# Kernel optimization log

Hardware: AMD Instinct MI355X
Metric: run time of the kernel (lower is better)

The kernel has to match this reference:

```python
import jax, jax.numpy as jnp
import numpy as np

H = 16  # num_attention_heads


def setup_inputs() -> dict:
    key = jax.random.key(0)
    ks = jax.random.split(key, 4)
    B, S, D = 2, 2048, 1024
    hidden_states = jax.random.normal(ks[0], (B, S, D), dtype=jnp.float32)
    attention_mask = jnp.zeros((B, 1, 1, S), dtype=jnp.float32)
    scale = 1.0 / np.sqrt(D)
    Wq = jax.random.normal(ks[1], (D, D), dtype=jnp.float32) * scale
    Wk = jax.random.normal(ks[2], (D, D), dtype=jnp.float32) * scale
    Wv = jax.random.normal(ks[3], (D, D), dtype=jnp.float32) * scale
    bq = jnp.zeros((D,), dtype=jnp.float32)
    bk = jnp.zeros((D,), dtype=jnp.float32)
    bv = jnp.zeros((D,), dtype=jnp.float32)
    return {"hidden_states": hidden_states, "attention_mask": attention_mask,
            "Wq": Wq, "bq": bq, "Wk": Wk, "bk": bk, "Wv": Wv, "bv": bv}


def reference(hidden_states, attention_mask, Wq, bq, Wk, bk, Wv, bv):
    B, S, D = hidden_states.shape
    Dh = D // H

    def proj(W, b):
        # torch Linear: x @ W.T + b ; reshape to [B, H, S, Dh]
        y = jnp.einsum('bsd,ed->bse', hidden_states, W) + b
        return y.reshape(B, S, H, Dh).transpose(0, 2, 1, 3)

    q = proj(Wq, bq)
    k = proj(Wk, bk)
    v = proj(Wv, bv)

    scores = jnp.einsum('bhqd,bhkd->bhqk', q, k) / jnp.sqrt(jnp.float32(Dh))
    scores = scores + attention_mask  # additive mask broadcast [B,1,1,S]
    probs = jax.nn.softmax(scores, axis=-1)  # [B,H,Sq,Sk]
    out_attention_scores = probs.sum(axis=-2).sum(axis=-2)  # [B, Sk]
    # dropout prob = 0 (eval) -> identity
    context = jnp.einsum('bhqk,bhkd->bhqd', probs, v)
    context = context.transpose(0, 2, 1, 3).reshape(B, S, D)
    return context, out_attention_scores
```

## Files before the change

kernel.cpp:

```cpp
#include <hip/hip_runtime.h>
#include <hip/hip_bf16.h>
#include <stdint.h>

typedef unsigned short u16;
typedef __attribute__((ext_vector_type(8))) unsigned short u16x8;
typedef __attribute__((ext_vector_type(4))) unsigned short u16x4;
typedef __attribute__((ext_vector_type(8))) __bf16 bf16x8;
typedef __attribute__((ext_vector_type(4))) float f32x4;
typedef __attribute__((ext_vector_type(16))) float f32x16;

#define LOG2E 1.44269504088896340736f

#if defined(__has_builtin)
#if __has_builtin(__builtin_amdgcn_exp2f)
#define EXP2(x) __builtin_amdgcn_exp2f(x)
#endif
#endif
#ifndef EXP2
#define EXP2(x) exp2f(x)
#endif

__device__ __forceinline__ f32x4 mfma16(u16x8 a, u16x8 b, f32x4 c) {
  return __builtin_amdgcn_mfma_f32_16x16x32_bf16(
      __builtin_bit_cast(bf16x8, a), __builtin_bit_cast(bf16x8, b), c, 0, 0, 0);
}

__device__ __forceinline__ f32x16 mfma32(u16x8 a, u16x8 b, f32x16 c) {
  return __builtin_amdgcn_mfma_f32_32x32x16_bf16(
      __builtin_bit_cast(bf16x8, a), __builtin_bit_cast(bf16x8, b), c, 0, 0, 0);
}

__device__ __forceinline__ u16 f2bf(float f) {
  unsigned u = __builtin_bit_cast(unsigned, f);
  return (u16)((u + 0x7fffu + ((u >> 16) & 1u)) >> 16);
}

__device__ __forceinline__ unsigned cvtpk(float a, float b) {
  unsigned r;
  asm volatile("v_cvt_pk_bf16_f32 %0, %1, %2" : "=v"(r) : "v"(a), "v"(b));
  return r;
}

__device__ __forceinline__ void pswap(unsigned& a, unsigned& b) {
  asm volatile("v_permlane32_swap_b32 %0, %1" : "+v"(a), "+v"(b));
}

__device__ __forceinline__ void gload_lds16(const void* g, void* l) {
  __builtin_amdgcn_global_load_lds(
      (__attribute__((address_space(1))) void*)const_cast<void*>(g),
      (__attribute__((address_space(3))) void*)l, 16, 0, 0);
}

template<int N> __device__ __forceinline__ void vmwait() {
  __builtin_amdgcn_sched_barrier(0);
  asm volatile("s_waitcnt vmcnt(%0)" :: "n"(N) : "memory");
  __builtin_amdgcn_sched_barrier(0);
}

#define SWZ(row, colbyte) ((((row) * 128) + (colbyte)) ^ (((row) & 7) << 4))

__global__ void cast_f32_bf16(const float* __restrict__ src, u16* __restrict__ dst, int n4) {
  int i = blockIdx.x * blockDim.x + threadIdx.x;
  if (i < n4) {
    f32x4 v = ((const f32x4*)src)[i];
    u16x4 o;
    o[0] = f2bf(v[0]); o[1] = f2bf(v[1]); o[2] = f2bf(v[2]); o[3] = f2bf(v[3]);
    ((u16x4*)dst)[i] = o;
  }
}

__global__ void cast3_f32_bf16(const float* __restrict__ s0, const float* __restrict__ s1,
                               const float* __restrict__ s2, u16* __restrict__ dst) {
  const int seg = blockIdx.x >> 10;
  const int i = (blockIdx.x & 1023) * blockDim.x + threadIdx.x;
  const float* src = (seg == 0) ? s0 : ((seg == 1) ? s1 : s2);
  f32x4 v = ((const f32x4*)src)[i];
  u16x4 o;
  o[0] = f2bf(v[0]); o[1] = f2bf(v[1]); o[2] = f2bf(v[2]); o[3] = f2bf(v[3]);
  ((u16x4*)(dst + (size_t)seg * 1048576))[i] = o;
}

__global__ __launch_bounds__(256) void gemm_qkv(
    const u16* __restrict__ A, const u16* __restrict__ Bm,
    const float* __restrict__ bq, const float* __restrict__ bk, const float* __restrict__ bv,
    u16* __restrict__ Qb, u16* __restrict__ Kb, u16* __restrict__ VTb) {
  __shared__ __align__(16) u16 Asm[3][4096];
  __shared__ __align__(16) u16 Bsm[3][4096];
  const int tid = threadIdx.x;
  const int wave = tid >> 6, lane = tid & 63;
  const int lq = lane & 15, lg = lane >> 4;
  const int wr = wave >> 1, wc = wave & 1;
  const int lin = blockIdx.y * 24 + blockIdx.x;
  const int wg = (lin & 7) * 96 + (lin >> 3);
  const int m0 = (wg / 24) * 128, n0 = (wg % 24) * 128;

  f32x4 zero = {0.f, 0.f, 0.f, 0.f};
  f32x4 acc[4][4];
#pragma unroll
  for (int mi = 0; mi < 4; ++mi)
#pragma unroll
    for (int ni = 0; ni < 4; ++ni) acc[mi][ni] = zero;

  auto stage = [&](int kt, int buf) {
    const int k0 = kt * 32;
#pragma unroll
    for (int c = 0; c < 2; ++c) {
      const int idx = wave * 2 + c;
      const u16* ga = A + (size_t)(m0 + idx * 16 + (lane >> 2)) * 1024 + k0 + (lane & 3) * 8;
      gload_lds16(ga, (char*)&Asm[buf][0] + idx * 1024);
      const u16* gb = Bm + (size_t)(n0 + idx * 16 + (lane >> 2)) * 1024 + k0 + (lane & 3) * 8;
      gload_lds16(gb, (char*)&Bsm[buf][0] + idx * 1024);
    }
  };

  stage(0, 0);
  stage(1, 1);
  for (int kt = 0; kt < 32; ++kt) {
    if (kt < 31) vmwait<4>(); else vmwait<0>();
    __builtin_amdgcn_s_barrier();
    if (kt + 2 < 32) stage(kt + 2, (kt + 2) % 3);
    const int cur = kt % 3;

    __builtin_amdgcn_s_setprio(1);
    u16x8 af[4], bfr[4];
#pragma unroll
    for (int mi = 0; mi < 4; ++mi)
      af[mi] = *(const u16x8*)&Asm[cur][(wr * 64 + mi * 16 + lq) * 32 + lg * 8];
#pragma unroll
    for (int ni = 0; ni < 4; ++ni)
      bfr[ni] = *(const u16x8*)&Bsm[cur][(wc * 64 + ni * 16 + lq) * 32 + lg * 8];
#pragma unroll
    for (int mi = 0; mi < 4; ++mi)
#pragma unroll
      for (int ni = 0; ni < 4; ++ni)
        acc[mi][ni] = mfma16(af[mi], bfr[ni], acc[mi][ni]);
    __builtin_amdgcn_s_setprio(0);
  }

  const int which = n0 >> 10;
  const float* bias = (which == 0) ? bq : ((which == 1) ? bk : bv);
  const float scl = (which == 0) ? (0.125f * LOG2E) : 1.0f;
#pragma unroll
  for (int mi = 0; mi < 4; ++mi) {
    const int m = m0 + wr * 64 + mi * 16 + lg * 4;
    const int bb = m >> 11;
    const int s = m & 2047;
#pragma unroll
    for (int ni = 0; ni < 4; ++ni) {
      const int n = n0 + wc * 64 + ni * 16 + lq;
      const int d = n & 1023;
      const int h = d >> 6, dh = d & 63;
      const float bi = bias[d];
#pragma unroll
      for (int r = 0; r < 4; ++r) {
        float v = (acc[mi][ni][r] + bi) * scl;
        if (which == 2)
          VTb[(((size_t)bb * 16 + h) * 64 + dh) * 2048 + (size_t)(s + r)] = f2bf(v);
        else {
          u16* dst = (which == 0) ? Qb : Kb;
          dst[(((size_t)bb * 16 + h) * 2048 + (size_t)(s + r)) * 64 + dh] = f2bf(v);
        }
      }
    }
  }
}

__global__ __launch_bounds__(512) void attn_pair(
    const u16* __restrict__ Qb, const u16* __restrict__ Kb, const u16* __restrict__ VTb,
    const float* __restrict__ maskg, float* __restrict__ out_ctx, float* __restrict__ winv) {
  __shared__ __align__(16) u16 Kl[2][2][4096];
  __shared__ __align__(16) u16 VTl[2][2][4096];

  const int tid = threadIdx.x;
  const int w = tid >> 6, lane = tid & 63;
  const int l31 = lane & 31, h = lane >> 5;
  const int hf = w >> 2, p = w & 3;
  const int bid = (blockIdx.x & 7) * 64 + (blockIdx.x >> 3);
  const int qt = bid & 15, bh = bid >> 4;
  const int b = bh >> 4, hh = bh & 15;
  const int qw = qt * 128 + p * 32;
  const int kt0 = hf * 16;

  const u16* qp = Qb + ((size_t)bh * 2048 + qw + l31) * 64 + h * 8;
  u16x8 qa[4];
#pragma unroll
  for (int dq = 0; dq < 4; ++dq) qa[dq] = *(const u16x8*)(qp + dq * 16);

  const char* Kbase = (const char*)(Kb + (size_t)bh * 2048 * 64);
  const char* VTbase = (const char*)(VTb + (size_t)bh * 64 * 2048);
  const float* mbase = maskg + b * 2048;

  const int t8 = tid & 255;
  const int srow = t8 >> 3;
  const int scol = ((t8 & 7) * 16) ^ ((srow & 7) << 4);
  auto stage = [&](int kt, int buf) {
    const char* ksrc = Kbase + (size_t)(kt * 64) * 128;
    char* kd = (char*)&Kl[hf][buf][0] + (w & 3) * 1024;
    gload_lds16(ksrc + (size_t)srow * 128 + scol, kd);
    gload_lds16(ksrc + (size_t)(srow + 32) * 128 + scol, kd + 4096);
    const char* vsrc = VTbase + (size_t)kt * 128;
    char* vd = (char*)&VTl[hf][buf][0] + (w & 3) * 1024;
    gload_lds16(vsrc + (size_t)srow * 4096 + scol, vd);
    gload_lds16(vsrc + (size_t)(srow + 32) * 4096 + scol, vd + 4096);
  };

  f32x16 accpv[2];
#pragma unroll
  for (int db = 0; db < 2; ++db)
#pragma unroll
    for (int r = 0; r < 16; ++r) accpv[db][r] = 0.f;
  float l_l = 0.f;

  stage(kt0, 0);
  for (int j = 0; j < 16; ++j) {
    const int kt = kt0 + j;
    vmwait<0>();
    __builtin_amdgcn_s_barrier();
    const int cur = j & 1;
    const char* Kt = (const char*)&Kl[hf][cur][0];
    const char* Vt = (const char*)&VTl[hf][cur][0];

    __builtin_amdgcn_s_setprio(1);
#pragma unroll
    for (int kb = 0; kb < 2; ++kb) {
      f32x16 s;
#pragma unroll
      for (int r = 0; r < 16; ++r) s[r] = 0.f;
#pragma unroll
      for (int dq = 0; dq < 4; ++dq) {
        const u16x8 ka = *(const u16x8*)(Kt + SWZ(kb * 32 + l31, dq * 32 + h * 16));
        s = mfma32(ka, qa[dq], s);
      }
      float pv[16];
#pragma unroll
      for (int g = 0; g < 4; ++g) {
        const f32x4 mv = *(const f32x4*)(mbase + kt * 64 + kb * 32 + g * 8 + h * 4);
#pragma unroll
        for (int j2 = 0; j2 < 4; ++j2)
          pv[g * 4 + j2] = EXP2(fmaf(mv[j2], LOG2E, s[g * 4 + j2]));
      }
      l_l += ((pv[0] + pv[1]) + (pv[2] + pv[3])) + ((pv[4] + pv[5]) + (pv[6] + pv[7])) +
             ((pv[8] + pv[9]) + (pv[10] + pv[11])) + ((pv[12] + pv[13]) + (pv[14] + pv[15]));
      unsigned a01 = cvtpk(pv[0], pv[1]), a23 = cvtpk(pv[2], pv[3]);
      unsigned a45 = cvtpk(pv[4], pv[5]), a67 = cvtpk(pv[6], pv[7]);
      unsigned b01 = cvtpk(pv[8], pv[9]), b23 = cvtpk(pv[10], pv[11]);
      unsigned b45 = cvtpk(pv[12], pv[13]), b67 = cvtpk(pv[14], pv[15]);
      pswap(a01, a45); pswap(a23, a67);
      pswap(b01, b45); pswap(b23, b67);
      uint4 f1 = {a01, a23, a45, a67};
      uint4 f2 = {b01, b23, b45, b67};
      u16x8 pf[2] = {__builtin_bit_cast(u16x8, f1), __builtin_bit_cast(u16x8, f2)};
#pragma unroll
      for (int ks2 = 0; ks2 < 2; ++ks2) {
#pragma unroll
        for (int db = 0; db < 2; ++db) {
          const u16x8 vt = *(const u16x8*)(Vt + SWZ(db * 32 + l31, kb * 64 + ks2 * 32 + h * 16));
          accpv[db] = mfma32(pf[ks2], vt, accpv[db]);
        }
      }
    }
    __builtin_amdgcn_s_setprio(0);
    __builtin_amdgcn_sched_barrier(0);
    if (j + 1 < 16) stage(kt0 + j + 1, cur ^ 1);
  }

  l_l += __shfl_xor(l_l, 32);

  __syncthreads();
  float* pairctx = (float*)&Kl[0][0][0];
  float* pairl   = (float*)&VTl[0][0][0];
  if (hf == 1) {
#pragma unroll
    for (int db = 0; db < 2; ++db)
#pragma unroll
      for (int r = 0; r < 16; ++r) {
        const int q = (r & 3) + (r >> 2) * 8 + h * 4;
        pairctx[p * 2048 + q * 64 + db * 32 + l31] = accpv[db][r];
      }
    if (h == 0) pairl[p * 32 + l31] = l_l;
  }
  __syncthreads();
  if (hf == 0) {
    const float lt = l_l + pairl[p * 32 + l31];
    const float il = 1.0f / lt;
    if (h == 0) winv[bh * 2048 + qw + l31] = il;
#pragma unroll
    for (int r = 0; r < 16; ++r) {
      const int q = (r & 3) + (r >> 2) * 8 + h * 4;
      const float ilr = __shfl(il, q);
      const size_t row = (size_t)(b * 2048 + qw + q) * 1024 + hh * 64;
      out_ctx[row + l31] =
          (accpv[0][r] + pairctx[p * 2048 + q * 64 + l31]) * ilr;
      out_ctx[row + 32 + l31] =
          (accpv[1][r] + pairctx[p * 2048 + q * 64 + 32 + l31]) * ilr;
    }
  }
}

__global__ __launch_bounds__(256) void colsum_kernel(
    const u16* __restrict__ Qb, const u16* __restrict__ Kb,
    const float* __restrict__ maskg, const float* __restrict__ winv,
    float* __restrict__ out_cs) {
  __shared__ __align__(16) u16 Ql[3][4096];

  const int tid = threadIdx.x;
  const int w = tid >> 6, lane = tid & 63;
  const int lq = lane & 15, lg = lane >> 4;
  const int bid = (blockIdx.x & 7) * 128 + (blockIdx.x >> 3);
  const int ktile = bid & 15, qh = (bid >> 4) & 1, bh = bid >> 5;
  const int b = bh >> 4;
  const int kbase = ktile * 128 + w * 32;
  const int q0t = qh * 16;

  const u16* kp0 = Kb + ((size_t)bh * 2048 + kbase + lq) * 64 + lg * 8;
  const u16* kp1 = kp0 + 16 * 64;
  const u16x8 kb00 = *(const u16x8*)kp0, kb01 = *(const u16x8*)(kp0 + 32);
  const u16x8 kb10 = *(const u16x8*)kp1, kb11 = *(const u16x8*)(kp1 + 32);
  const float mvl0 = maskg[b * 2048 + kbase + lq] * LOG2E;
  const float mvl1 = maskg[b * 2048 + kbase + 16 + lq] * LOG2E;
  const float* wbase = winv + bh * 2048;
  const char* Qbase = (const char*)(Qb + (size_t)bh * 2048 * 64);

  const int r0 = tid >> 3;
  const int scol = ((tid & 7) * 16) ^ ((r0 & 7) << 4);
  auto stageQ = [&](int qt, int buf) {
    const char* src = Qbase + (size_t)(qt * 64) * 128;
    char* d = (char*)&Ql[buf][0] + w * 1024;
    gload_lds16(src + (size_t)r0 * 128 + scol, d);
    gload_lds16(src + (size_t)(r0 + 32) * 128 + scol, d + 4096);
  };

  float c0 = 0.f, c1 = 0.f;
  stageQ(q0t, 0);
  stageQ(q0t + 1, 1);
  for (int j = 0; j < 16; ++j) {
    const int qt = q0t + j;
    if (j < 15) vmwait<2>(); else vmwait<0>();
    __builtin_amdgcn_s_barrier();
    const char* Qt = (const char*)&Ql[j % 3][0];
    __builtin_amdgcn_s_setprio(1);
#pragma unroll
    for (int chunk = 0; chunk < 4; ++chunk) {
      const u16x8 qf0 = *(const u16x8*)(Qt + SWZ(chunk * 16 + lq, lg * 16));
      const u16x8 qf1 = *(const u16x8*)(Qt + SWZ(chunk * 16 + lq, 64 + lg * 16));
      f32x4 z = {0.f, 0.f, 0.f, 0.f};
      f32x4 s0 = mfma16(qf0, kb00, z);
      s0 = mfma16(qf1, kb01, s0);
      f32x4 s1 = mfma16(qf0, kb10, z);
      s1 = mfma16(qf1, kb11, s1);
      const f32x4 wv = *(const f32x4*)(wbase + qt * 64 + chunk * 16 + lg * 4);
#pragma unroll
      for (int r = 0; r < 4; ++r) {
        c0 += EXP2(s0[r] + mvl0) * wv[r];
        c1 += EXP2(s1[r] + mvl1) * wv[r];
      }
    }
    __builtin_amdgcn_s_setprio(0);
    __builtin_amdgcn_sched_barrier(0);
    if (j + 2 < 16) stageQ(q0t + j + 2, (j + 2) % 3);
  }
  c0 += __shfl_xor(c0, 16); c0 += __shfl_xor(c0, 32);
  c1 += __shfl_xor(c1, 16); c1 += __shfl_xor(c1, 32);
  if (lg == 0) {
    atomicAdd(&out_cs[b * 2048 + kbase + lq], c0);
    atomicAdd(&out_cs[b * 2048 + kbase + 16 + lq], c1);
  }
}

extern "C" void kernel_launch(void* const* d_in, const int* in_sizes, int n_in,
                              void* d_out, int out_size, void* d_ws, size_t ws_size,
                              hipStream_t stream) {
  (void)in_sizes; (void)n_in; (void)out_size; (void)ws_size;
  const float* X    = (const float*)d_in[0];
  const float* mask = (const float*)d_in[1];
  const float* Wq   = (const float*)d_in[2];
  const float* bq   = (const float*)d_in[3];
  const float* Wk   = (const float*)d_in[4];
  const float* bk   = (const float*)d_in[5];
  const float* Wv   = (const float*)d_in[6];
  const float* bv   = (const float*)d_in[7];
  float* out = (float*)d_out;

  char* ws = (char*)d_ws;
  u16* Xb   = (u16*)(ws);
  u16* Wcat = (u16*)(ws + 8388608);
  u16* Qb   = (u16*)(ws + 14680064);
  u16* Kb   = (u16*)(ws + 23068672);
  u16* VTb  = (u16*)(ws + 31457280);
  float* winv = (float*)(ws + 39845888);

  hipMemsetAsync(out + 4194304, 0, 4096 * sizeof(float), stream);

  cast_f32_bf16<<<4096, 256, 0, stream>>>(X, Xb, 1048576);
  cast3_f32_bf16<<<3072, 256, 0, stream>>>(Wq, Wk, Wv, Wcat);

  gemm_qkv<<<dim3(24, 32), 256, 0, stream>>>(Xb, Wcat, bq, bk, bv, Qb, Kb, VTb);

  attn_pair<<<512, 512, 0, stream>>>(Qb, Kb, VTb, mask, out, winv);
  colsum_kernel<<<1024, 256, 0, stream>>>(Qb, Kb, mask, winv, out + 4194304);
}
```

Baseline: 147.1 us.

## Merge cast kernels, swizzle GEMM LDS tiles, triple-buffer attention with smaller K tiles

Folds the X and weight fp32-to-bf16 cast launches into one kernel to save a launch. Changes the GEMM's LDS staging to an XOR-swizzled layout to cut bank conflicts on fragment reads. In the attention kernel, shrinks each key tile from 64 to 32, moves from double to triple buffering with two loads in flight, and swizzles the V^T tile in a packed two-rows-per-line layout. This trades more loop iterations and barriers for deeper prefetch and fewer LDS conflicts.

```diff
diff --git a/kernel.cpp b/kernel.cpp
--- a/kernel.cpp
+++ b/kernel.cpp
@@ -59,25 +59,28 @@
 
 #define SWZ(row, colbyte) ((((row) * 128) + (colbyte)) ^ (((row) & 7) << 4))
 
-__global__ void cast_f32_bf16(const float* __restrict__ src, u16* __restrict__ dst, int n4) {
-  int i = blockIdx.x * blockDim.x + threadIdx.x;
-  if (i < n4) {
-    f32x4 v = ((const f32x4*)src)[i];
-    u16x4 o;
-    o[0] = f2bf(v[0]); o[1] = f2bf(v[1]); o[2] = f2bf(v[2]); o[3] = f2bf(v[3]);
-    ((u16x4*)dst)[i] = o;
-  }
-}
-
-__global__ void cast3_f32_bf16(const float* __restrict__ s0, const float* __restrict__ s1,
-                               const float* __restrict__ s2, u16* __restrict__ dst) {
-  const int seg = blockIdx.x >> 10;
-  const int i = (blockIdx.x & 1023) * blockDim.x + threadIdx.x;
-  const float* src = (seg == 0) ? s0 : ((seg == 1) ? s1 : s2);
+__global__ void cast_all(const float* __restrict__ X,
+                         const float* __restrict__ s0, const float* __restrict__ s1,
+                         const float* __restrict__ s2,
+                         u16* __restrict__ Xb, u16* __restrict__ Wcat) {
+  const int bid = blockIdx.x;
+  const float* src;
+  u16* dst;
+  int i;
+  if (bid < 4096) {
+    src = X; dst = Xb;
+    i = bid * 256 + threadIdx.x;
+  } else {
+    const int wb = bid - 4096;
+    const int seg = wb >> 10;
+    src = (seg == 0) ? s0 : ((seg == 1) ? s1 : s2);
+    dst = Wcat + (size_t)seg * 1048576;
+    i = (wb & 1023) * 256 + threadIdx.x;
+  }
   f32x4 v = ((const f32x4*)src)[i];
   u16x4 o;
   o[0] = f2bf(v[0]); o[1] = f2bf(v[1]); o[2] = f2bf(v[2]); o[3] = f2bf(v[3]);
-  ((u16x4*)(dst + (size_t)seg * 1048576))[i] = o;
+  ((u16x4*)dst)[i] = o;
 }
 
 __global__ __launch_bounds__(256) void gemm_qkv(
@@ -101,16 +104,26 @@
 #pragma unroll
     for (int ni = 0; ni < 4; ++ni) acc[mi][ni] = zero;
 
+  int rA0, k16A0, rA1, k16A1;
+  {
+    const int cc0 = wave * 128 + lane;
+    const int ln0 = cc0 >> 3, sp0 = (cc0 & 7) ^ (ln0 & 7);
+    rA0 = ln0 * 2 + (sp0 >> 2); k16A0 = sp0 & 3;
+    const int cc1 = cc0 + 64;
+    const int ln1 = cc1 >> 3, sp1 = (cc1 & 7) ^ (ln1 & 7);
+    rA1 = ln1 * 2 + (sp1 >> 2); k16A1 = sp1 & 3;
+  }
+
   auto stage = [&](int kt, int buf) {
-    const int k0 = kt * 32;
-#pragma unroll
-    for (int c = 0; c < 2; ++c) {
-      const int idx = wave * 2 + c;
-      const u16* ga = A + (size_t)(m0 + idx * 16 + (lane >> 2)) * 1024 + k0 + (lane & 3) * 8;
-      gload_lds16(ga, (char*)&Asm[buf][0] + idx * 1024);
-      const u16* gb = Bm + (size_t)(n0 + idx * 16 + (lane >> 2)) * 1024 + k0 + (lane & 3) * 8;
-      gload_lds16(gb, (char*)&Bsm[buf][0] + idx * 1024);
-    }
+    const int kk = kt * 32;
+    gload_lds16(A + (size_t)(m0 + rA0) * 1024 + kk + k16A0 * 8,
+                (char*)&Asm[buf][0] + (wave * 2 + 0) * 1024);
+    gload_lds16(A + (size_t)(m0 + rA1) * 1024 + kk + k16A1 * 8,
+                (char*)&Asm[buf][0] + (wave * 2 + 1) * 1024);
+    gload_lds16(Bm + (size_t)(n0 + rA0) * 1024 + kk + k16A0 * 8,
+                (char*)&Bsm[buf][0] + (wave * 2 + 0) * 1024);
+    gload_lds16(Bm + (size_t)(n0 + rA1) * 1024 + kk + k16A1 * 8,
+                (char*)&Bsm[buf][0] + (wave * 2 + 1) * 1024);
   };
 
   stage(0, 0);
@@ -124,11 +137,21 @@
     __builtin_amdgcn_s_setprio(1);
     u16x8 af[4], bfr[4];
 #pragma unroll
-    for (int mi = 0; mi < 4; ++mi)
-      af[mi] = *(const u16x8*)&Asm[cur][(wr * 64 + mi * 16 + lq) * 32 + lg * 8];
-#pragma unroll
-    for (int ni = 0; ni < 4; ++ni)
-      bfr[ni] = *(const u16x8*)&Bsm[cur][(wc * 64 + ni * 16 + lq) * 32 + lg * 8];
+    for (int mi = 0; mi < 4; ++mi) {
+      const int rA = wr * 64 + mi * 16 + lq;
+      const int lnA = rA >> 1;
+      const int spA = ((rA & 1) << 2) | lg;
+      af[mi] = *(const u16x8*)((const char*)&Asm[cur][0] +
+                               lnA * 128 + ((spA ^ (lnA & 7)) << 4));
+    }
+#pragma unroll
+    for (int ni = 0; ni < 4; ++ni) {
+      const int rB = wc * 64 + ni * 16 + lq;
+      const int lnB = rB >> 1;
+      const int spB = ((rB & 1) << 2) | lg;
+      bfr[ni] = *(const u16x8*)((const char*)&Bsm[cur][0] +
+                                lnB * 128 + ((spB ^ (lnB & 7)) << 4));
+    }
 #pragma unroll
     for (int mi = 0; mi < 4; ++mi)
 #pragma unroll
@@ -168,8 +191,7 @@
 __global__ __launch_bounds__(512) void attn_pair(
     const u16* __restrict__ Qb, const u16* __restrict__ Kb, const u16* __restrict__ VTb,
     const float* __restrict__ maskg, float* __restrict__ out_ctx, float* __restrict__ winv) {
-  __shared__ __align__(16) u16 Kl[2][2][4096];
-  __shared__ __align__(16) u16 VTl[2][2][4096];
+  __shared__ __align__(16) char smem[49664];
 
   const int tid = threadIdx.x;
   const int w = tid >> 6, lane = tid & 63;
@@ -179,29 +201,29 @@
   const int qt = bid & 15, bh = bid >> 4;
   const int b = bh >> 4, hh = bh & 15;
   const int qw = qt * 128 + p * 32;
-  const int kt0 = hf * 16;
 
   const u16* qp = Qb + ((size_t)bh * 2048 + qw + l31) * 64 + h * 8;
   u16x8 qa[4];
 #pragma unroll
   for (int dq = 0; dq < 4; ++dq) qa[dq] = *(const u16x8*)(qp + dq * 16);
 
-  const char* Kbase = (const char*)(Kb + (size_t)bh * 2048 * 64);
-  const char* VTbase = (const char*)(VTb + (size_t)bh * 64 * 2048);
+  const char* KbaseG = (const char*)(Kb + (size_t)bh * 2048 * 64);
+  const char* VTbaseG = (const char*)(VTb + (size_t)bh * 64 * 2048);
   const float* mbase = maskg + b * 2048;
 
   const int t8 = tid & 255;
-  const int srow = t8 >> 3;
-  const int scol = ((t8 & 7) * 16) ^ ((srow & 7) << 4);
+  const int srowK = t8 >> 3;
+  const int scolK = ((t8 & 7) * 16) ^ ((srowK & 7) << 4);
+  const int lineV = t8 >> 3;
+  const int spV = (t8 & 7) ^ (lineV & 7);
+  const int dhV = lineV * 2 + (spV >> 2);
+  const int kbV = (spV & 3) * 16;
+
   auto stage = [&](int kt, int buf) {
-    const char* ksrc = Kbase + (size_t)(kt * 64) * 128;
-    char* kd = (char*)&Kl[hf][buf][0] + (w & 3) * 1024;
-    gload_lds16(ksrc + (size_t)srow * 128 + scol, kd);
-    gload_lds16(ksrc + (size_t)(srow + 32) * 128 + scol, kd + 4096);
-    const char* vsrc = VTbase + (size_t)kt * 128;
-    char* vd = (char*)&VTl[hf][buf][0] + (w & 3) * 1024;
-    gload_lds16(vsrc + (size_t)srow * 4096 + scol, vd);
-    gload_lds16(vsrc + (size_t)(srow + 32) * 4096 + scol, vd + 4096);
+    char* kd = smem + hf * 12288 + buf * 4096 + (w & 3) * 1024;
+    gload_lds16(KbaseG + (size_t)(kt * 32 + srowK) * 128 + scolK, kd);
+    char* vd = smem + 24576 + hf * 12288 + buf * 4096 + (w & 3) * 1024;
+    gload_lds16(VTbaseG + (size_t)dhV * 4096 + (size_t)kt * 64 + kbV, vd);
   };
 
   f32x16 accpv[2];
@@ -211,64 +233,65 @@
     for (int r = 0; r < 16; ++r) accpv[db][r] = 0.f;
   float l_l = 0.f;
 
+  const int kt0 = hf * 32;
   stage(kt0, 0);
-  for (int j = 0; j < 16; ++j) {
+  stage(kt0 + 1, 1);
+  for (int j = 0; j < 32; ++j) {
     const int kt = kt0 + j;
-    vmwait<0>();
+    if (j < 31) vmwait<2>(); else vmwait<0>();
     __builtin_amdgcn_s_barrier();
-    const int cur = j & 1;
-    const char* Kt = (const char*)&Kl[hf][cur][0];
-    const char* Vt = (const char*)&VTl[hf][cur][0];
+    const char* Kt = smem + hf * 12288 + (j % 3) * 4096;
+    const char* Vt = smem + 24576 + hf * 12288 + (j % 3) * 4096;
 
     __builtin_amdgcn_s_setprio(1);
-#pragma unroll
-    for (int kb = 0; kb < 2; ++kb) {
-      f32x16 s;
-#pragma unroll
-      for (int r = 0; r < 16; ++r) s[r] = 0.f;
-#pragma unroll
-      for (int dq = 0; dq < 4; ++dq) {
-        const u16x8 ka = *(const u16x8*)(Kt + SWZ(kb * 32 + l31, dq * 32 + h * 16));
-        s = mfma32(ka, qa[dq], s);
-      }
-      float pv[16];
-#pragma unroll
-      for (int g = 0; g < 4; ++g) {
-        const f32x4 mv = *(const f32x4*)(mbase + kt * 64 + kb * 32 + g * 8 + h * 4);
-#pragma unroll
-        for (int j2 = 0; j2 < 4; ++j2)
-          pv[g * 4 + j2] = EXP2(fmaf(mv[j2], LOG2E, s[g * 4 + j2]));
-      }
-      l_l += ((pv[0] + pv[1]) + (pv[2] + pv[3])) + ((pv[4] + pv[5]) + (pv[6] + pv[7])) +
-             ((pv[8] + pv[9]) + (pv[10] + pv[11])) + ((pv[12] + pv[13]) + (pv[14] + pv[15]));
-      unsigned a01 = cvtpk(pv[0], pv[1]), a23 = cvtpk(pv[2], pv[3]);
-      unsigned a45 = cvtpk(pv[4], pv[5]), a67 = cvtpk(pv[6], pv[7]);
-      unsigned b01 = cvtpk(pv[8], pv[9]), b23 = cvtpk(pv[10], pv[11]);
-      unsigned b45 = cvtpk(pv[12], pv[13]), b67 = cvtpk(pv[14], pv[15]);
-      pswap(a01, a45); pswap(a23, a67);
-      pswap(b01, b45); pswap(b23, b67);
-      uint4 f1 = {a01, a23, a45, a67};
-      uint4 f2 = {b01, b23, b45, b67};
-      u16x8 pf[2] = {__builtin_bit_cast(u16x8, f1), __builtin_bit_cast(u16x8, f2)};
-#pragma unroll
-      for (int ks2 = 0; ks2 < 2; ++ks2) {
-#pragma unroll
-        for (int db = 0; db < 2; ++db) {
-          const u16x8 vt = *(const u16x8*)(Vt + SWZ(db * 32 + l31, kb * 64 + ks2 * 32 + h * 16));
-          accpv[db] = mfma32(pf[ks2], vt, accpv[db]);
-        }
+    f32x16 s;
+#pragma unroll
+    for (int r = 0; r < 16; ++r) s[r] = 0.f;
+#pragma unroll
+    for (int dq = 0; dq < 4; ++dq) {
+      const u16x8 ka = *(const u16x8*)(Kt + SWZ(l31, dq * 32 + h * 16));
+      s = mfma32(ka, qa[dq], s);
+    }
+    float pv[16];
+#pragma unroll
+    for (int g = 0; g < 4; ++g) {
+      const f32x4 mv = *(const f32x4*)(mbase + kt * 32 + g * 8 + h * 4);
+#pragma unroll
+      for (int j2 = 0; j2 < 4; ++j2)
+        pv[g * 4 + j2] = EXP2(fmaf(mv[j2], LOG2E, s[g * 4 + j2]));
+    }
+    l_l += ((pv[0] + pv[1]) + (pv[2] + pv[3])) + ((pv[4] + pv[5]) + (pv[6] + pv[7])) +
+           ((pv[8] + pv[9]) + (pv[10] + pv[11])) + ((pv[12] + pv[13]) + (pv[14] + pv[15]));
+    unsigned a01 = cvtpk(pv[0], pv[1]), a23 = cvtpk(pv[2], pv[3]);
+    unsigned a45 = cvtpk(pv[4], pv[5]), a67 = cvtpk(pv[6], pv[7]);
+    unsigned b01 = cvtpk(pv[8], pv[9]), b23 = cvtpk(pv[10], pv[11]);
+    unsigned b45 = cvtpk(pv[12], pv[13]), b67 = cvtpk(pv[14], pv[15]);
+    pswap(a01, a45); pswap(a23, a67);
+    pswap(b01, b45); pswap(b23, b67);
+    uint4 f1 = {a01, a23, a45, a67};
+    uint4 f2 = {b01, b23, b45, b67};
+    u16x8 pf[2] = {__builtin_bit_cast(u16x8, f1), __builtin_bit_cast(u16x8, f2)};
+#pragma unroll
+    for (int ks2 = 0; ks2 < 2; ++ks2) {
+#pragma unroll
+      for (int db = 0; db < 2; ++db) {
+        const int rowV = db * 32 + l31;
+        const int lnV = rowV >> 1;
+        const int sV = ((rowV & 1) << 2) | (ks2 << 1) | h;
+        const u16x8 vt = *(const u16x8*)(Vt + lnV * 128 + ((sV ^ (lnV & 7)) << 4));
+        accpv[db] = mfma32(pf[ks2], vt, accpv[db]);
       }
     }
     __builtin_amdgcn_s_setprio(0);
     __builtin_amdgcn_sched_barrier(0);
-    if (j + 1 < 16) stage(kt0 + j + 1, cur ^ 1);
+    if (j + 2 < 32) stage(kt0 + j + 2, (j + 2) % 3);
   }
 
   l_l += __shfl_xor(l_l, 32);
 
   __syncthreads();
-  float* pairctx = (float*)&Kl[0][0][0];
-  float* pairl   = (float*)&VTl[0][0][0];
+  float* pairctx = (float*)smem;
+  float* pairl = (float*)(smem + 49152);
   if (hf == 1) {
 #pragma unroll
     for (int db = 0; db < 2; ++db)
@@ -289,10 +312,8 @@
       const int q = (r & 3) + (r >> 2) * 8 + h * 4;
       const float ilr = __shfl(il, q);
       const size_t row = (size_t)(b * 2048 + qw + q) * 1024 + hh * 64;
-      out_ctx[row + l31] =
-          (accpv[0][r] + pairctx[p * 2048 + q * 64 + l31]) * ilr;
-      out_ctx[row + 32 + l31] =
-          (accpv[1][r] + pairctx[p * 2048 + q * 64 + 32 + l31]) * ilr;
+      out_ctx[row + l31] = (accpv[0][r] + pairctx[p * 2048 + q * 64 + l31]) * ilr;
+      out_ctx[row + 32 + l31] = (accpv[1][r] + pairctx[p * 2048 + q * 64 + 32 + l31]) * ilr;
     }
   }
 }
@@ -391,8 +412,7 @@
 
   hipMemsetAsync(out + 4194304, 0, 4096 * sizeof(float), stream);
 
-  cast_f32_bf16<<<4096, 256, 0, stream>>>(X, Xb, 1048576);
-  cast3_f32_bf16<<<3072, 256, 0, stream>>>(Wq, Wk, Wv, Wcat);
+  cast_all<<<7168, 256, 0, stream>>>(X, Wq, Wk, Wv, Xb, Wcat);
 
   gemm_qkv<<<dim3(24, 32), 256, 0, stream>>>(Xb, Wcat, bq, bk, bv, Qb, Kb, VTb);
 
```

Result: faster. 143.2 us (-2.6%).
